# Optimization experiments

Hardware: AMD Instinct MI355X
Metric: run time of the kernel (lower is better)

## Reference

```python
import jax, jax.numpy as jnp
import numpy as np

B, F, V, D, K = 16384, 39, 30000, 16, 20
EPS = 1e-5


def bn_eval(x, g, b):
    # inference-mode BatchNorm1d with running_mean=0, running_var=1
    return g * x / jnp.sqrt(1.0 + EPS) + b


def setup_inputs() -> dict:
    key = jax.random.key(0)
    ks = jax.random.split(key, 12)
    x = jax.random.randint(ks[0], (B, F), 0, V)
    emb_table = jax.random.normal(ks[1], (F * V, D), dtype=jnp.float32) * 0.05
    w_c = jax.random.normal(ks[2], (F, F * D), dtype=jnp.float32) * 0.05
    w0 = jax.random.normal(ks[3], (1024, F * D), dtype=jnp.float32) * 0.04
    w1 = jax.random.normal(ks[4], (512, 1024), dtype=jnp.float32) * 0.03
    w_out = jax.random.normal(ks[5], (1, 512), dtype=jnp.float32) * 0.04
    return {
        'x': x, 'emb_table': emb_table,
        'w_c': w_c, 'b_c': jnp.zeros((F,)), 'g_c': jnp.ones((F,)), 'be_c': jnp.zeros((F,)),
        'w0': w0, 'b0': jnp.zeros((1024,)), 'g0': jnp.ones((1024,)), 'be0': jnp.zeros((1024,)),
        'w1': w1, 'b1': jnp.zeros((512,)), 'g1': jnp.ones((512,)), 'be1': jnp.zeros((512,)),
        'w_out': w_out, 'b_out': jnp.zeros((1,)),
    }


def reference(x, emb_table, w_c, b_c, g_c, be_c, w0, b0, g0, be0,
              w1, b1, g1, be1, w_out, b_out):
    offsets = jnp.arange(F, dtype=x.dtype) * V          # per-field offsets
    idx = x + offsets[None, :]                          # [B, F]
    emb = emb_table[idx]                                # [B, F, D] gather

    # controller_mlp: flatten (batch, D, F) layout like torch transpose(1,2)
    flat = jnp.transpose(emb, (0, 2, 1)).reshape(B, F * D)
    h = jax.nn.relu(bn_eval(flat @ w_c.T + b_c, g_c, be_c))
    scores = jax.nn.softmax(h, axis=1)                  # [B, F]

    # kmax_pooling: top-k field indices, sorted ascending, gather weights
    _, kidx = jax.lax.top_k(scores, K)
    kidx = jnp.sort(kidx, axis=1)                       # [B, K]
    w = jnp.take_along_axis(scores, kidx, axis=1)       # [B, K]

    # forward_select: gather selected field embeddings, weight them
    sel = jnp.take_along_axis(emb, kidx[:, :, None], axis=1)  # [B, K, D]
    weighted = sel * w[:, :, None]

    # scatter back into full field slots (unselected fields are zero)
    full = jnp.zeros((B, F, D), weighted.dtype)
    bidx = jnp.arange(B)[:, None]
    full = full.at[bidx, kidx].set(weighted)            # [B, F, D]

    z = jnp.transpose(full, (0, 2, 1)).reshape(B, F * D)
    z = jax.nn.relu(bn_eval(z @ w0.T + b0, g0, be0))
    z = jax.nn.relu(bn_eval(z @ w1.T + b1, g1, be1))
    out = jax.nn.sigmoid(z @ w_out.T + b_out)           # [B, 1]
    return out.squeeze(-1)
```

## Files before the change

kernel.cpp:

```cpp
#include <hip/hip_runtime.h>
#include <math.h>

#define B_SZ 16384
#define F_N 39
#define V_N 30000
#define D_N 16
#define K_SEL 20
#define FD 624
#define KP0 640
#define NCP 48
#define N0 1024
#define N1 512
#define CBR 16
#define ALD 648

typedef unsigned short u16;
typedef __attribute__((ext_vector_type(8))) short bf16x8;
typedef __attribute__((ext_vector_type(8))) unsigned short u16x8;
typedef __attribute__((ext_vector_type(4))) float f32x4;
typedef __attribute__((ext_vector_type(4))) unsigned short u16x4;

__device__ __forceinline__ u16 f2bf(float v) {
    union { float f; unsigned u; } x; x.f = v;
    unsigned r = x.u + 0x7fff + ((x.u >> 16) & 1);
    return (u16)(r >> 16);
}
__device__ __forceinline__ float bf2f(u16 v) {
    union { unsigned u; float f; } x; x.u = ((unsigned)v) << 16;
    return x.f;
}

#define GLD16(gp, lp) __builtin_amdgcn_global_load_lds( \
    (const __attribute__((address_space(1))) unsigned int*)(gp), \
    (__attribute__((address_space(3))) unsigned int*)(lp), 16, 0, 0)

#define PREP_W0 (N0 * KP0)
#define PREP_W1 (N1 * N0)
#define PREP_WC (NCP * KP0)
#define PREP_TOT (PREP_W0 + PREP_W1 + PREP_WC + 3 * NCP + B_SZ)

__global__ __launch_bounds__(256) void prep_all_kernel(
    const float* __restrict__ w0, const float* __restrict__ w1,
    const float* __restrict__ w_c, const float* __restrict__ b_c,
    const float* __restrict__ g_c, const float* __restrict__ be_c,
    u16* __restrict__ w0b, u16* __restrict__ w1b, u16* __restrict__ wcb,
    float* __restrict__ bcp, float* __restrict__ gcp, float* __restrict__ becp,
    float* __restrict__ outp)
{
    int i = blockIdx.x * blockDim.x + threadIdx.x;
    if (i < PREP_W0) {
        int n = i / KP0, kk = i - n * KP0;
        float v = 0.f;
        if (kk < FD) v = w0[n * FD + (kk & 15) * F_N + (kk >> 4)];
        w0b[i] = f2bf(v);
        return;
    }
    i -= PREP_W0;
    if (i < PREP_W1) { w1b[i] = f2bf(w1[i]); return; }
    i -= PREP_W1;
    if (i < PREP_WC) {
        int n = i / KP0, kk = i - n * KP0;
        float v = 0.f;
        if (n < F_N && kk < FD) v = w_c[n * FD + (kk & 15) * F_N + (kk >> 4)];
        wcb[i] = f2bf(v);
        return;
    }
    i -= PREP_WC;
    if (i < 3 * NCP) {
        int which = i / NCP, n = i - which * NCP;
        float v = 0.f;
        if (n < F_N) v = (which == 0) ? b_c[n] : (which == 1) ? g_c[n] : be_c[n];
        ((which == 0) ? bcp : (which == 1) ? gcp : becp)[n] = v;
        return;
    }
    i -= 3 * NCP;
    if (i < B_SZ) outp[i] = 0.f;
}

__global__ __launch_bounds__(256) void fused_controller_kernel(
    const int* __restrict__ x, const float* __restrict__ emb_table,
    const u16* __restrict__ wcb, const float* __restrict__ bcp,
    const float* __restrict__ gcp, const float* __restrict__ becp,
    u16* __restrict__ zb)
{
    __shared__ __align__(16) u16 Al[CBR * ALD];
    __shared__ float vv[CBR][49];
    __shared__ f32x4 part[4][64][3];
    __shared__ float selw[CBR][F_N];

    const int t    = threadIdx.x;
    const int wave = t >> 6;
    const int lane = t & 63;
    const int b0   = blockIdx.x * CBR;

    {
        const int p0 = t, p1 = t + 256, p2 = t + 512;
        const int xi0 = x[b0 * F_N + p0];
        const int xi1 = x[b0 * F_N + p1];
        const int xi2 = (p2 < CBR * F_N) ? x[b0 * F_N + p2] : 0;
        const int pp[3] = { p0, p1, p2 };
        const int xx[3] = { xi0, xi1, xi2 };
        #pragma unroll
        for (int s = 0; s < 3; ++s) {
            const int p = pp[s];
            if (p < CBR * F_N) {
                const int row = p / F_N;
                const int f   = p - row * F_N;
                const float4* src =
                    (const float4*)(emb_table + (size_t)(xx[s] + f * V_N) * D_N);
                float4 v0 = src[0], v1 = src[1], v2 = src[2], v3 = src[3];
                u16x8 o0 = { f2bf(v0.x), f2bf(v0.y), f2bf(v0.z), f2bf(v0.w),
                             f2bf(v1.x), f2bf(v1.y), f2bf(v1.z), f2bf(v1.w) };
                u16x8 o1 = { f2bf(v2.x), f2bf(v2.y), f2bf(v2.z), f2bf(v2.w),
                             f2bf(v3.x), f2bf(v3.y), f2bf(v3.z), f2bf(v3.w) };
                *(u16x8*)&Al[row * ALD + f * D_N]     = o0;
                *(u16x8*)&Al[row * ALD + f * D_N + 8] = o1;
            }
        }
    }
    __syncthreads();

    const int m = lane & 15;
    const int q = lane >> 4;
    f32x4 acc0 = {}, acc1 = {}, acc2 = {};
    {
        const u16* ap  = &Al[m * ALD + wave * 160 + q * 8];
        const u16* bp0 = wcb + (size_t)(0  + m) * KP0 + wave * 160 + q * 8;
        const u16* bp1 = wcb + (size_t)(16 + m) * KP0 + wave * 160 + q * 8;
        const u16* bp2 = wcb + (size_t)(32 + m) * KP0 + wave * 160 + q * 8;
        #pragma unroll
        for (int k = 0; k < 5; ++k) {
            bf16x8 af = *(const bf16x8*)ap;
            bf16x8 b0 = *(const bf16x8*)bp0;
            bf16x8 b1 = *(const bf16x8*)bp1;
            bf16x8 b2 = *(const bf16x8*)bp2;
            acc0 = __builtin_amdgcn_mfma_f32_16x16x32_bf16(af, b0, acc0, 0, 0, 0);
            acc1 = __builtin_amdgcn_mfma_f32_16x16x32_bf16(af, b1, acc1, 0, 0, 0);
            acc2 = __builtin_amdgcn_mfma_f32_16x16x32_bf16(af, b2, acc2, 0, 0, 0);
            ap += 32; bp0 += 32; bp1 += 32; bp2 += 32;
        }
    }
    part[wave][lane][0] = acc0;
    part[wave][lane][1] = acc1;
    part[wave][lane][2] = acc2;
    __syncthreads();

    {
        f32x4 r0 = part[0][lane][0] + part[1][lane][0] + part[2][lane][0] + part[3][lane][0];
        f32x4 r1 = part[0][lane][1] + part[1][lane][1] + part[2][lane][1] + part[3][lane][1];
        f32x4 r2 = part[0][lane][2] + part[1][lane][2] + part[2][lane][2] + part[3][lane][2];

        const float rs = rsqrtf(1.0f + 1e-5f);
        if (q == wave) {
            #pragma unroll
            for (int j = 0; j < 3; ++j) {
                const f32x4 a = (j == 0) ? r0 : (j == 1) ? r1 : r2;
                const int n = j * 16 + m;
                const float gn = gcp[n] * rs;
                const float bn = becp[n];
                const float bi = bcp[n];
                #pragma unroll
                for (int r = 0; r < 4; ++r)
                    vv[wave * 4 + r][n] = fmaxf(fmaf(gn, a[r] + bi, bn), 0.f);
            }
        }
    }
    __syncthreads();

    {
        const int row = wave * 4 + (lane >> 4);
        const int fl  = lane & 15;
        float e[3] = {0.f, 0.f, 0.f};
        float mloc = -1e30f;
        #pragma unroll
        for (int it = 0; it < 3; ++it) {
            const int f = fl + 16 * it;
            if (f < F_N) { e[it] = vv[row][f]; mloc = fmaxf(mloc, e[it]); }
        }
        mloc = fmaxf(mloc, __shfl_xor(mloc, 1, 64));
        mloc = fmaxf(mloc, __shfl_xor(mloc, 2, 64));
        mloc = fmaxf(mloc, __shfl_xor(mloc, 4, 64));
        mloc = fmaxf(mloc, __shfl_xor(mloc, 8, 64));
        float sloc = 0.f;
        #pragma unroll
        for (int it = 0; it < 3; ++it) {
            const int f = fl + 16 * it;
            if (f < F_N) { e[it] = expf(e[it] - mloc); sloc += e[it]; }
        }
        sloc += __shfl_xor(sloc, 1, 64);
        sloc += __shfl_xor(sloc, 2, 64);
        sloc += __shfl_xor(sloc, 4, 64);
        sloc += __shfl_xor(sloc, 8, 64);
        const float inv = 1.f / sloc;
        #pragma unroll
        for (int it = 0; it < 3; ++it) {
            const int f = fl + 16 * it;
            if (f < F_N) vv[row][f] = e[it];
        }

        int rank[3] = {};
        for (int gg = 0; gg < F_N; ++gg) {
            const float o = vv[row][gg];
            #pragma unroll
            for (int it = 0; it < 3; ++it) {
                const int f = fl + 16 * it;
                if (f < F_N)
                    rank[it] += (o > e[it] || (o == e[it] && gg < f)) ? 1 : 0;
            }
        }
        #pragma unroll
        for (int it = 0; it < 3; ++it) {
            const int f = fl + 16 * it;
            if (f < F_N)
                selw[row][f] = (rank[it] < K_SEL) ? e[it] * inv : 0.f;
        }
    }
    __syncthreads();

    for (int gp = t; gp < CBR * 40; gp += 256) {
        const int row  = gp / 40;
        const int slot = gp - row * 40;
        u16* dst = zb + (size_t)(b0 + row) * KP0 + slot * D_N;
        u16x8 o0 = {0,0,0,0,0,0,0,0}, o1 = {0,0,0,0,0,0,0,0};
        if (slot < F_N) {
            const float w = selw[row][slot];
            u16x8 a0 = *(u16x8*)&Al[row * ALD + slot * D_N];
            u16x8 a1 = *(u16x8*)&Al[row * ALD + slot * D_N + 8];
            #pragma unroll
            for (int k = 0; k < 8; ++k) {
                o0[k] = f2bf(bf2f(a0[k]) * w);
                o1[k] = f2bf(bf2f(a1[k]) * w);
            }
        }
        *(u16x8*)dst = o0;
        *(u16x8*)(dst + 8) = o1;
    }
}

template<int MODE>
__global__ __launch_bounds__(256) void gemm_mfma_bn_relu(
    const u16* __restrict__ A, const u16* __restrict__ W,
    const float* __restrict__ bias, const float* __restrict__ g,
    const float* __restrict__ be, u16* __restrict__ Cout,
    int M, int N, int Kp,
    const float* __restrict__ w_out, float* __restrict__ outp)
{
    __shared__ __align__(16) u16 SM[6 * 4096];
    u16* const As0 = SM;
    u16* const Bs0 = SM + 3 * 4096;

    const int t    = threadIdx.x;
    const int wave = t >> 6;
    const int lane = t & 63;
    const int wm   = wave >> 1, wn = wave & 1;
    const int m0   = blockIdx.x * 128;
    const int n0   = blockIdx.y * 128;

    const int lr    = lane >> 2;
    const int swz_u = (lane & 3) ^ ((lane >> 3) & 3);
    const u16* gA = A + (size_t)(m0 + wave * 32 + lr) * Kp + swz_u * 8;
    const u16* gB = W + (size_t)(n0 + wave * 32 + lr) * Kp + swz_u * 8;
    const size_t kstep16 = 16 * (size_t)Kp;
    const int oA0 = (wave * 32) * 32;
    const int oA1 = (wave * 32 + 16) * 32;

    const int q    = lane >> 4;
    const int lr16 = lane & 15;

    int aoff[4], boff[4];
    #pragma unroll
    for (int i = 0; i < 4; ++i) {
        int ra = wm * 64 + i * 16 + lr16;
        aoff[i] = ra * 32 + ((q ^ ((ra >> 1) & 3)) * 8);
        int rb = wn * 64 + i * 16 + lr16;
        boff[i] = rb * 32 + ((q ^ ((rb >> 1) & 3)) * 8);
    }

    const int NIT = Kp >> 5;

    GLD16(gA,           As0 + oA0);
    GLD16(gA + kstep16, As0 + oA1);
    GLD16(gB,           Bs0 + oA0);
    GLD16(gB + kstep16, Bs0 + oA1);
    gA += 32; gB += 32;
    GLD16(gA,           As0 + 4096 + oA0);
    GLD16(gA + kstep16, As0 + 4096 + oA1);
    GLD16(gB,           Bs0 + 4096 + oA0);
    GLD16(gB + kstep16, Bs0 + 4096 + oA1);
    gA += 32; gB += 32;

    f32x4 acc[4][4] = {};
    int cur = 0, stg = 2;

    for (int it = 0; it < NIT - 1; ++it) {
        asm volatile("s_waitcnt vmcnt(4)" ::: "memory");
        __builtin_amdgcn_s_barrier();
        __builtin_amdgcn_sched_barrier(0);

        if (it + 2 < NIT) {
            u16* as = As0 + stg * 4096;
            u16* bs = Bs0 + stg * 4096;
            GLD16(gA,           as + oA0);
            GLD16(gA + kstep16, as + oA1);
            GLD16(gB,           bs + oA0);
            GLD16(gB + kstep16, bs + oA1);
            gA += 32; gB += 32;
        }

        const u16* ac = As0 + cur * 4096;
        const u16* bc = Bs0 + cur * 4096;
        bf16x8 af[4], bfr[4];
        #pragma unroll
        for (int i = 0; i < 4; ++i) af[i]  = *(const bf16x8*)(ac + aoff[i]);
        #pragma unroll
        for (int j = 0; j < 4; ++j) bfr[j] = *(const bf16x8*)(bc + boff[j]);

        __builtin_amdgcn_s_setprio(1);
        #pragma unroll
        for (int i = 0; i < 4; ++i)
            #pragma unroll
            for (int j = 0; j < 4; ++j)
                acc[i][j] = __builtin_amdgcn_mfma_f32_16x16x32_bf16(
                    af[i], bfr[j], acc[i][j], 0, 0, 0);
        __builtin_amdgcn_s_setprio(0);

        cur = (cur == 2) ? 0 : cur + 1;
        stg = (stg == 2) ? 0 : stg + 1;
    }

    asm volatile("s_waitcnt vmcnt(0)" ::: "memory");
    __builtin_amdgcn_s_barrier();
    __builtin_amdgcn_sched_barrier(0);
    {
        const u16* ac = As0 + cur * 4096;
        const u16* bc = Bs0 + cur * 4096;
        bf16x8 af[4], bfr[4];
        #pragma unroll
        for (int i = 0; i < 4; ++i) af[i]  = *(const bf16x8*)(ac + aoff[i]);
        #pragma unroll
        for (int j = 0; j < 4; ++j) bfr[j] = *(const bf16x8*)(bc + boff[j]);
        __builtin_amdgcn_s_setprio(1);
        #pragma unroll
        for (int i = 0; i < 4; ++i)
            #pragma unroll
            for (int j = 0; j < 4; ++j)
                acc[i][j] = __builtin_amdgcn_mfma_f32_16x16x32_bf16(
                    af[i], bfr[j], acc[i][j], 0, 0, 0);
        __builtin_amdgcn_s_setprio(0);
    }

    const float rs = rsqrtf(1.0f + 1e-5f);
    if (MODE == 0) {
        __syncthreads();
        u16* Cs = SM;
        #pragma unroll
        for (int j = 0; j < 4; ++j) {
            const int nl = wn * 64 + j * 16 + lr16;
            const int n  = n0 + nl;
            const float bn_g = g[n] * rs;
            const float bn_b = be[n];
            const float bi   = bias[n];
            #pragma unroll
            for (int i = 0; i < 4; ++i) {
                const int ml = wm * 64 + i * 16 + q * 4;
                #pragma unroll
                for (int r = 0; r < 4; ++r) {
                    float v = acc[i][j][r] + bi;
                    Cs[(ml + r) * 136 + nl] =
                        f2bf(fmaxf(fmaf(bn_g, v, bn_b), 0.f));
                }
            }
        }
        __syncthreads();
        #pragma unroll
        for (int s = 0; s < 8; ++s) {
            const int chunk = s * 256 + t;
            const int row   = chunk >> 4;
            const int col   = (chunk & 15) << 3;
            *(u16x8*)&Cout[(size_t)(m0 + row) * N + n0 + col] =
                *(const u16x8*)&Cs[row * 136 + col];
        }
    } else {
        float s[4][4] = {};
        #pragma unroll
        for (int j = 0; j < 4; ++j) {
            const int n = n0 + wn * 64 + j * 16 + lr16;
            const float bn_g = g[n] * rs;
            const float bn_b = be[n];
            const float bi   = bias[n];
            const float wo   = w_out[n];
            #pragma unroll
            for (int i = 0; i < 4; ++i)
                #pragma unroll
                for (int r = 0; r < 4; ++r) {
                    float v = acc[i][j][r] + bi;
                    v = fmaxf(fmaf(bn_g, v, bn_b), 0.f);
                    s[i][r] = fmaf(v, wo, s[i][r]);
                }
        }
        #pragma unroll
        for (int i = 0; i < 4; ++i)
            #pragma unroll
            for (int r = 0; r < 4; ++r) {
                float v = s[i][r];
                v += __shfl_xor(v, 1, 64);
                v += __shfl_xor(v, 2, 64);
                v += __shfl_xor(v, 4, 64);
                v += __shfl_xor(v, 8, 64);
                s[i][r] = v;
            }
        if (lr16 == 0) {
            #pragma unroll
            for (int i = 0; i < 4; ++i) {
                const int mbase = m0 + wm * 64 + i * 16 + q * 4;
                #pragma unroll
                for (int r = 0; r < 4; ++r)
                    atomicAdd(&outp[mbase + r], s[i][r]);
            }
        }
    }
}

__global__ __launch_bounds__(256) void sigmoid_kernel(
    const float* __restrict__ outp, const float* __restrict__ b_out,
    float* __restrict__ out)
{
    const int b = blockIdx.x * 256 + threadIdx.x;
    out[b] = 1.f / (1.f + expf(-(outp[b] + b_out[0])));
}

extern "C" void kernel_launch(void* const* d_in, const int* in_sizes, int n_in,
                              void* d_out, int out_size, void* d_ws, size_t ws_size,
                              hipStream_t stream)
{
    const int*   x     = (const int*)  d_in[0];
    const float* emb   = (const float*)d_in[1];
    const float* w_c   = (const float*)d_in[2];
    const float* b_c   = (const float*)d_in[3];
    const float* g_c   = (const float*)d_in[4];
    const float* be_c  = (const float*)d_in[5];
    const float* w0    = (const float*)d_in[6];
    const float* b0    = (const float*)d_in[7];
    const float* g0    = (const float*)d_in[8];
    const float* be0   = (const float*)d_in[9];
    const float* w1    = (const float*)d_in[10];
    const float* b1    = (const float*)d_in[11];
    const float* g1    = (const float*)d_in[12];
    const float* be1   = (const float*)d_in[13];
    const float* w_out = (const float*)d_in[14];
    const float* b_out = (const float*)d_in[15];
    float* out = (float*)d_out;

    u16*   zb    = (u16*)d_ws;
    u16*   w0b   = zb    + (size_t)B_SZ * KP0;
    u16*   h0b   = w0b   + (size_t)N0 * KP0;
    u16*   w1b   = h0b   + (size_t)B_SZ * N0;
    u16*   wcb   = w1b   + (size_t)N1 * N0;
    float* outp  = (float*)(wcb + (size_t)NCP * KP0);
    float* bcp   = outp + B_SZ;
    float* gcp   = bcp + NCP;
    float* becp  = gcp + NCP;

    prep_all_kernel<<<(PREP_TOT + 255) / 256, 256, 0, stream>>>(
        w0, w1, w_c, b_c, g_c, be_c, w0b, w1b, wcb, bcp, gcp, becp, outp);

    fused_controller_kernel<<<B_SZ / CBR, 256, 0, stream>>>(
        x, emb, wcb, bcp, gcp, becp, zb);

    gemm_mfma_bn_relu<0><<<dim3(B_SZ / 128, N0 / 128), 256, 0, stream>>>(
        zb, w0b, b0, g0, be0, h0b, B_SZ, N0, KP0, nullptr, nullptr);

    gemm_mfma_bn_relu<1><<<dim3(B_SZ / 128, N1 / 128), 256, 0, stream>>>(
        h0b, w1b, b1, g1, be1, nullptr, B_SZ, N1, N0, w_out, outp);

    sigmoid_kernel<<<B_SZ / 256, 256, 0, stream>>>(outp, b_out, out);
}
```

Before: 211.4 us.

## Enlarge GEMM block tile to 256x128 with 512 threads, use packed bf16 conversion

Each GEMM block now covers 256 rows instead of 128 and runs 8 waves. Each B tile is therefore reused across twice as many A rows, and the LDS staging is rearranged into a unified 3-stage buffer with one load per operand slice per thread. Separately, the manual round-to-nearest fp32-to-bf16 conversions in the controller and the epilogue are replaced with the hardware v_cvt_pk_bf16_f32 instruction. The larger block uses more LDS (72 KB) and halves the number of blocks, which may reduce occupancy and load balance.

```diff
diff --git a/kernel.cpp b/kernel.cpp
--- a/kernel.cpp
+++ b/kernel.cpp
@@ -28,6 +28,11 @@
 __device__ __forceinline__ float bf2f(u16 v) {
     union { unsigned u; float f; } x; x.u = ((unsigned)v) << 16;
     return x.f;
+}
+__device__ __forceinline__ unsigned cvtpk2(float a, float b) {
+    unsigned d;
+    asm("v_cvt_pk_bf16_f32 %0, %1, %2" : "=v"(d) : "v"(a), "v"(b));
+    return d;
 }
 
 #define GLD16(gp, lp) __builtin_amdgcn_global_load_lds( \
@@ -109,12 +114,12 @@
                 const float4* src =
                     (const float4*)(emb_table + (size_t)(xx[s] + f * V_N) * D_N);
                 float4 v0 = src[0], v1 = src[1], v2 = src[2], v3 = src[3];
-                u16x8 o0 = { f2bf(v0.x), f2bf(v0.y), f2bf(v0.z), f2bf(v0.w),
-                             f2bf(v1.x), f2bf(v1.y), f2bf(v1.z), f2bf(v1.w) };
-                u16x8 o1 = { f2bf(v2.x), f2bf(v2.y), f2bf(v2.z), f2bf(v2.w),
-                             f2bf(v3.x), f2bf(v3.y), f2bf(v3.z), f2bf(v3.w) };
-                *(u16x8*)&Al[row * ALD + f * D_N]     = o0;
-                *(u16x8*)&Al[row * ALD + f * D_N + 8] = o1;
+                uint4 o0 = { cvtpk2(v0.x, v0.y), cvtpk2(v0.z, v0.w),
+                             cvtpk2(v1.x, v1.y), cvtpk2(v1.z, v1.w) };
+                uint4 o1 = { cvtpk2(v2.x, v2.y), cvtpk2(v2.z, v2.w),
+                             cvtpk2(v3.x, v3.y), cvtpk2(v3.z, v3.w) };
+                *(uint4*)&Al[row * ALD + f * D_N]     = o0;
+                *(uint4*)&Al[row * ALD + f * D_N + 8] = o1;
             }
         }
     }
@@ -221,48 +226,50 @@
         const int row  = gp / 40;
         const int slot = gp - row * 40;
         u16* dst = zb + (size_t)(b0 + row) * KP0 + slot * D_N;
-        u16x8 o0 = {0,0,0,0,0,0,0,0}, o1 = {0,0,0,0,0,0,0,0};
+        uint4 o0 = {0u,0u,0u,0u}, o1 = {0u,0u,0u,0u};
         if (slot < F_N) {
             const float w = selw[row][slot];
             u16x8 a0 = *(u16x8*)&Al[row * ALD + slot * D_N];
             u16x8 a1 = *(u16x8*)&Al[row * ALD + slot * D_N + 8];
-            #pragma unroll
-            for (int k = 0; k < 8; ++k) {
-                o0[k] = f2bf(bf2f(a0[k]) * w);
-                o1[k] = f2bf(bf2f(a1[k]) * w);
-            }
-        }
-        *(u16x8*)dst = o0;
-        *(u16x8*)(dst + 8) = o1;
+            o0 = (uint4){ cvtpk2(bf2f(a0[0]) * w, bf2f(a0[1]) * w),
+                          cvtpk2(bf2f(a0[2]) * w, bf2f(a0[3]) * w),
+                          cvtpk2(bf2f(a0[4]) * w, bf2f(a0[5]) * w),
+                          cvtpk2(bf2f(a0[6]) * w, bf2f(a0[7]) * w) };
+            o1 = (uint4){ cvtpk2(bf2f(a1[0]) * w, bf2f(a1[1]) * w),
+                          cvtpk2(bf2f(a1[2]) * w, bf2f(a1[3]) * w),
+                          cvtpk2(bf2f(a1[4]) * w, bf2f(a1[5]) * w),
+                          cvtpk2(bf2f(a1[6]) * w, bf2f(a1[7]) * w) };
+        }
+        *(uint4*)dst       = o0;
+        *(uint4*)(dst + 8) = o1;
     }
 }
 
 template<int MODE>
-__global__ __launch_bounds__(256) void gemm_mfma_bn_relu(
+__global__ __launch_bounds__(512) void gemm_mfma_bn_relu(
     const u16* __restrict__ A, const u16* __restrict__ W,
     const float* __restrict__ bias, const float* __restrict__ g,
     const float* __restrict__ be, u16* __restrict__ Cout,
     int M, int N, int Kp,
     const float* __restrict__ w_out, float* __restrict__ outp)
 {
-    __shared__ __align__(16) u16 SM[6 * 4096];
-    u16* const As0 = SM;
-    u16* const Bs0 = SM + 3 * 4096;
+    __shared__ __align__(16) u16 SM[3 * 12288];
 
     const int t    = threadIdx.x;
     const int wave = t >> 6;
     const int lane = t & 63;
     const int wm   = wave >> 1, wn = wave & 1;
-    const int m0   = blockIdx.x * 128;
+    const int m0   = blockIdx.x * 256;
     const int n0   = blockIdx.y * 128;
 
-    const int lr    = lane >> 2;
-    const int swz_u = (lane & 3) ^ ((lane >> 3) & 3);
-    const u16* gA = A + (size_t)(m0 + wave * 32 + lr) * Kp + swz_u * 8;
-    const u16* gB = W + (size_t)(n0 + wave * 32 + lr) * Kp + swz_u * 8;
-    const size_t kstep16 = 16 * (size_t)Kp;
-    const int oA0 = (wave * 32) * 32;
-    const int oA1 = (wave * 32 + 16) * 32;
+    const int rA0 = t >> 2;
+    const int cA0 = (t & 3) ^ ((rA0 >> 1) & 3);
+    const int rA1 = 128 + rA0;
+    const int cA1 = (t & 3) ^ ((rA1 >> 1) & 3);
+    const u16* gA0 = A + (size_t)(m0 + rA0) * Kp + cA0 * 8;
+    const u16* gA1 = A + (size_t)(m0 + rA1) * Kp + cA1 * 8;
+    const u16* gB  = W + (size_t)(n0 + rA0) * Kp + cA0 * 8;
+    const int dA0 = t * 8, dA1 = 4096 + t * 8, dB = 8192 + t * 8;
 
     const int q    = lane >> 4;
     const int lr16 = lane & 15;
@@ -278,37 +285,33 @@
 
     const int NIT = Kp >> 5;
 
-    GLD16(gA,           As0 + oA0);
-    GLD16(gA + kstep16, As0 + oA1);
-    GLD16(gB,           Bs0 + oA0);
-    GLD16(gB + kstep16, Bs0 + oA1);
-    gA += 32; gB += 32;
-    GLD16(gA,           As0 + 4096 + oA0);
-    GLD16(gA + kstep16, As0 + 4096 + oA1);
-    GLD16(gB,           Bs0 + 4096 + oA0);
-    GLD16(gB + kstep16, Bs0 + 4096 + oA1);
-    gA += 32; gB += 32;
+    GLD16(gA0, SM + dA0);
+    GLD16(gA1, SM + dA1);
+    GLD16(gB,  SM + dB);
+    gA0 += 32; gA1 += 32; gB += 32;
+    GLD16(gA0, SM + 12288 + dA0);
+    GLD16(gA1, SM + 12288 + dA1);
+    GLD16(gB,  SM + 12288 + dB);
+    gA0 += 32; gA1 += 32; gB += 32;
 
     f32x4 acc[4][4] = {};
     int cur = 0, stg = 2;
 
     for (int it = 0; it < NIT - 1; ++it) {
-        asm volatile("s_waitcnt vmcnt(4)" ::: "memory");
+        asm volatile("s_waitcnt vmcnt(3)" ::: "memory");
         __builtin_amdgcn_s_barrier();
         __builtin_amdgcn_sched_barrier(0);
 
         if (it + 2 < NIT) {
-            u16* as = As0 + stg * 4096;
-            u16* bs = Bs0 + stg * 4096;
-            GLD16(gA,           as + oA0);
-            GLD16(gA + kstep16, as + oA1);
-            GLD16(gB,           bs + oA0);
-            GLD16(gB + kstep16, bs + oA1);
-            gA += 32; gB += 32;
-        }
-
-        const u16* ac = As0 + cur * 4096;
-        const u16* bc = Bs0 + cur * 4096;
+            u16* s = SM + stg * 12288;
+            GLD16(gA0, s + dA0);
+            GLD16(gA1, s + dA1);
+            GLD16(gB,  s + dB);
+            gA0 += 32; gA1 += 32; gB += 32;
+        }
+
+        const u16* ac = SM + cur * 12288;
+        const u16* bc = ac + 8192;
         bf16x8 af[4], bfr[4];
         #pragma unroll
         for (int i = 0; i < 4; ++i) af[i]  = *(const bf16x8*)(ac + aoff[i]);
@@ -332,8 +335,8 @@
     __builtin_amdgcn_s_barrier();
     __builtin_amdgcn_sched_barrier(0);
     {
-        const u16* ac = As0 + cur * 4096;
-        const u16* bc = Bs0 + cur * 4096;
+        const u16* ac = SM + cur * 12288;
+        const u16* bc = ac + 8192;
         bf16x8 af[4], bfr[4];
         #pragma unroll
         for (int i = 0; i < 4; ++i) af[i]  = *(const bf16x8*)(ac + aoff[i]);
@@ -362,19 +365,23 @@
             const float bi   = bias[n];
             #pragma unroll
             for (int i = 0; i < 4; ++i) {
-                const int ml = wm * 64 + i * 16 + q * 4;
-                #pragma unroll
-                for (int r = 0; r < 4; ++r) {
-                    float v = acc[i][j][r] + bi;
-                    Cs[(ml + r) * 136 + nl] =
-                        f2bf(fmaxf(fmaf(bn_g, v, bn_b), 0.f));
-                }
+                const int mlb = wm * 64 + i * 16 + q * 4;
+                float v0 = fmaxf(fmaf(bn_g, acc[i][j][0] + bi, bn_b), 0.f);
+                float v1 = fmaxf(fmaf(bn_g, acc[i][j][1] + bi, bn_b), 0.f);
+                float v2 = fmaxf(fmaf(bn_g, acc[i][j][2] + bi, bn_b), 0.f);
+                float v3 = fmaxf(fmaf(bn_g, acc[i][j][3] + bi, bn_b), 0.f);
+                unsigned pA = cvtpk2(v0, v1);
+                unsigned pB = cvtpk2(v2, v3);
+                Cs[(mlb + 0) * 136 + nl] = (u16)pA;
+                Cs[(mlb + 1) * 136 + nl] = (u16)(pA >> 16);
+                Cs[(mlb + 2) * 136 + nl] = (u16)pB;
+                Cs[(mlb + 3) * 136 + nl] = (u16)(pB >> 16);
             }
         }
         __syncthreads();
         #pragma unroll
         for (int s = 0; s < 8; ++s) {
-            const int chunk = s * 256 + t;
+            const int chunk = s * 512 + t;
             const int row   = chunk >> 4;
             const int col   = (chunk & 15) << 3;
             *(u16x8*)&Cout[(size_t)(m0 + row) * N + n0 + col] =
@@ -467,10 +474,10 @@
     fused_controller_kernel<<<B_SZ / CBR, 256, 0, stream>>>(
         x, emb, wcb, bcp, gcp, becp, zb);
 
-    gemm_mfma_bn_relu<0><<<dim3(B_SZ / 128, N0 / 128), 256, 0, stream>>>(
+    gemm_mfma_bn_relu<0><<<dim3(B_SZ / 256, N0 / 128), 512, 0, stream>>>(
         zb, w0b, b0, g0, be0, h0b, B_SZ, N0, KP0, nullptr, nullptr);
 
-    gemm_mfma_bn_relu<1><<<dim3(B_SZ / 128, N1 / 128), 256, 0, stream>>>(
+    gemm_mfma_bn_relu<1><<<dim3(B_SZ / 256, N1 / 128), 512, 0, stream>>>(
         h0b, w1b, b1, g1, be1, nullptr, B_SZ, N1, N0, w_out, outp);
 
     sigmoid_kernel<<<B_SZ / 256, 256, 0, stream>>>(outp, b_out, out);
```

Result: faster. 207.2 us (-2.0%).
